# Kernel tuning notes

Measured on AMD Instinct MI355X. Metric: run time of the kernel, lower is better.

Reference implementation:

```python
import jax, jax.numpy as jnp
import numpy as np
import math

B, S, D, H = 1, 4096, 1024, 16
DH = D // H  # head_dim = 64
NEG = -10000.0  # matches torch masked-fill value in source (not -inf)


def setup_inputs() -> dict:
    key = jax.random.key(0)
    ks = jax.random.split(key, 5)
    scale = 0.02
    return {
        "x": jax.random.normal(ks[0], (B, S, D), dtype=jnp.float32),
        "Wqkv_w": jax.random.normal(ks[1], (3 * D, D), dtype=jnp.float32) * scale,
        "Wqkv_b": jax.random.normal(ks[2], (3 * D,), dtype=jnp.float32) * scale,
        "out_w": jax.random.normal(ks[3], (D, D), dtype=jnp.float32) * scale,
        "out_b": jax.random.normal(ks[4], (D,), dtype=jnp.float32) * scale,
    }


def reference(x, Wqkv_w, Wqkv_b, out_w, out_b):
    # QKV projection: (B,S,D) @ (D,3D) + b -> (B,S,3,H,DH)
    qkv = jnp.einsum('bsd,ed->bse', x, Wqkv_w) + Wqkv_b
    qkv = qkv.reshape(B, S, 3, H, DH)
    q, k, v = qkv[:, :, 0], qkv[:, :, 1], qkv[:, :, 2]  # each (B,S,H,DH)
    softmax_scale = 1.0 / math.sqrt(DH)
    # scores: (B,H,T,S)
    scores = jnp.einsum('bthd,bshd->bhts', q, k * softmax_scale)
    # causal additive mask with -10000 above diagonal (faithful to source)
    causal_mask = jnp.triu(jnp.full((S, S), NEG, dtype=scores.dtype), k=1)
    scores = scores + causal_mask
    attention = jax.nn.softmax(scores, axis=-1)
    context = jnp.einsum('bhts,bshd->bthd', attention, v)  # (B,T,H,DH)
    context = context.reshape(B, S, D)
    out = jnp.einsum('bsd,ed->bse', context, out_w) + out_b
    return out
```

## Files before the change

kernel.cpp:

```cpp
#include <hip/hip_runtime.h>
#include <hip/hip_bf16.h>

using f32x4  = __attribute__((ext_vector_type(4))) float;
using f32x16 = __attribute__((ext_vector_type(16))) float;
using bf16x8 = __attribute__((ext_vector_type(8))) __bf16;
using u16x8  = __attribute__((ext_vector_type(8))) unsigned short;
using u32x4  = __attribute__((ext_vector_type(4))) unsigned int;

#define DEV __device__ __forceinline__

constexpr int S_  = 4096;
constexpr int D_  = 1024;
constexpr int KD  = 1024;

constexpr size_t XB_OFF   = 0;
constexpr size_t WQKV_OFF = 8388608;
constexpr size_t WOUT_OFF = 14680064;
constexpr size_t QB_OFF   = 16777216;
constexpr size_t KB_OFF   = 25165824;
constexpr size_t VT_OFF   = 33554432;
constexpr size_t CTX_OFF  = 41943040;

DEV unsigned short f2bf(float f) {
  __hip_bfloat16 h = __float2bfloat16(f);
  return __builtin_bit_cast(unsigned short, h);
}

DEV void gl_lds16(const void* g, void* l) {
  __builtin_amdgcn_global_load_lds(
      (const __attribute__((address_space(1))) void*)g,
      (__attribute__((address_space(3))) void*)l, 16, 0, 0);
}

DEV f32x4 mfma16(bf16x8 a, bf16x8 b, f32x4 c) {
  return __builtin_amdgcn_mfma_f32_16x16x32_bf16(a, b, c, 0, 0, 0);
}
DEV f32x16 mfma32(bf16x8 a, bf16x8 b, f32x16 c) {
  return __builtin_amdgcn_mfma_f32_32x32x16_bf16(a, b, c, 0, 0, 0);
}
DEV unsigned cvtpk(float lo, float hi) {
  unsigned r;
  asm("v_cvt_pk_bf16_f32 %0, %1, %2" : "=v"(r) : "v"(lo), "v"(hi));
  return r;
}
DEV float exp2_fast(float x) {
  float r;
  asm("v_exp_f32 %0, %1" : "=v"(r) : "v"(x));
  return r;
}
DEV void pl32(unsigned& a, unsigned& b) {
  asm("v_permlane32_swap_b32 %0, %1" : "+v"(a), "+v"(b));
}
DEV float xhalf_max(float x) {
  float y;
  asm("v_mov_b32 %0, %1" : "=v"(y) : "v"(x));
  unsigned a = __builtin_bit_cast(unsigned, x), b = __builtin_bit_cast(unsigned, y);
  pl32(a, b);
  return fmaxf(__builtin_bit_cast(float, a), __builtin_bit_cast(float, b));
}
DEV float xhalf_add(float x) {
  float y;
  asm("v_mov_b32 %0, %1" : "=v"(y) : "v"(x));
  unsigned a = __builtin_bit_cast(unsigned, x), b = __builtin_bit_cast(unsigned, y);
  pl32(a, b);
  return __builtin_bit_cast(float, a) + __builtin_bit_cast(float, b);
}

__global__ void cvt_k(const float* __restrict__ s, unsigned short* __restrict__ d, int n8) {
  int i = blockIdx.x * 256 + threadIdx.x;
  if (i >= n8) return;
  const float4* s4 = (const float4*)s;
  float4 a = s4[2 * i], b = s4[2 * i + 1];
  u16x8 o;
  o[0] = f2bf(a.x); o[1] = f2bf(a.y); o[2] = f2bf(a.z); o[3] = f2bf(a.w);
  o[4] = f2bf(b.x); o[5] = f2bf(b.y); o[6] = f2bf(b.z); o[7] = f2bf(b.w);
  ((u16x8*)d)[i] = o;
}

template <int EPI>
__global__ __launch_bounds__(256)
void gemm_bt_k(const unsigned short* __restrict__ A,
               const unsigned short* __restrict__ Bt,
               const float* __restrict__ bias,
               unsigned short* __restrict__ qb,
               unsigned short* __restrict__ kb,
               unsigned short* __restrict__ vt,
               float* __restrict__ outf) {
  __shared__ unsigned short As[128 * 32];
  __shared__ unsigned short Bs[128 * 32];
  const int t = threadIdx.x;
  const int w = t >> 6, l = t & 63;
  const int lr = l & 15, lg = l >> 4, lk = lg * 8;
  const int m0 = blockIdx.y * 128, n0 = blockIdx.x * 128;
  const int wm = (w >> 1) * 64, wn = (w & 1) * 64;

  f32x4 acc[4][4] = {};

  const int srow = t >> 2;
  const int scolb = (t & 3) << 4;
  const char* Ag = (const char*)A + (size_t)(m0 + srow) * (KD * 2) + scolb;
  const char* Bg = (const char*)Bt + (size_t)(n0 + srow) * (KD * 2) + scolb;
  char* AsB = (char*)As;
  char* BsB = (char*)Bs;

  for (int kt = 0; kt < KD / 32; ++kt) {
    const char* ak = Ag + kt * 64;
    const char* bk = Bg + kt * 64;
    gl_lds16(ak,                 AsB + t * 16);
    gl_lds16(ak + 64 * (KD * 2), AsB + 4096 + t * 16);
    gl_lds16(bk,                 BsB + t * 16);
    gl_lds16(bk + 64 * (KD * 2), BsB + 4096 + t * 16);
    __syncthreads();

    bf16x8 a[4], b[4];
#pragma unroll
    for (int mi = 0; mi < 4; ++mi)
      a[mi] = *(const bf16x8*)&As[(wm + mi * 16 + lr) * 32 + lk];
#pragma unroll
    for (int ni = 0; ni < 4; ++ni)
      b[ni] = *(const bf16x8*)&Bs[(wn + ni * 16 + lr) * 32 + lk];
#pragma unroll
    for (int mi = 0; mi < 4; ++mi)
#pragma unroll
      for (int ni = 0; ni < 4; ++ni)
        acc[mi][ni] = mfma16(a[mi], b[ni], acc[mi][ni]);
    __syncthreads();
  }

  const int r0 = lg * 4;
  if (EPI == 0) {
    const int which = n0 >> 10;
    const float kscale = 0.125f * 1.44269504088896f;
#pragma unroll
    for (int mi = 0; mi < 4; ++mi) {
      const int sbase = m0 + wm + mi * 16 + r0;
#pragma unroll
      for (int ni = 0; ni < 4; ++ni) {
        const int e = n0 + wn + ni * 16 + lr;
        const float bv = bias[e];
        const int h = (e & 1023) >> 6, dd = e & 63;
#pragma unroll
        for (int r = 0; r < 4; ++r) {
          const float v = acc[mi][ni][r] + bv;
          const int sr = sbase + r;
          if (which == 0)      qb[((size_t)(h * S_ + sr)) * 64 + dd] = f2bf(v);
          else if (which == 1) kb[((size_t)(h * S_ + sr)) * 64 + dd] = f2bf(v * kscale);
          else                 vt[((size_t)(h * 64 + dd)) * S_ + sr] = f2bf(v);
        }
      }
    }
  } else {
#pragma unroll
    for (int mi = 0; mi < 4; ++mi) {
      const int sbase = m0 + wm + mi * 16 + r0;
#pragma unroll
      for (int ni = 0; ni < 4; ++ni) {
        const int e = n0 + wn + ni * 16 + lr;
        const float bv = bias[e];
#pragma unroll
        for (int r = 0; r < 4; ++r)
          outf[(size_t)(sbase + r) * D_ + e] = acc[mi][ni][r] + bv;
      }
    }
  }
}

__global__ __launch_bounds__(512, 2)
void attn_k(const unsigned short* __restrict__ Qb,
            const unsigned short* __restrict__ Kb,
            const unsigned short* __restrict__ Vt,
            unsigned short* __restrict__ ctx) {
  __shared__ char smem[65536];

  const int t = threadIdx.x;
  const int w8 = t >> 6;
  const int g  = w8 >> 2;
  const int w  = w8 & 3;
  const int l = t & 63, lq = l & 31, hi = l >> 5;
  const int pairIdx = blockIdx.x;
  const int h = blockIdx.y;

  const int sg = t >> 8;
  const int ts = t & 255;
  const int srow = ts >> 3;
  const int ssw  = ((ts & 7) << 4) ^ ((srow & 7) << 4);
  const char* Kg0 = (const char*)Kb + (size_t)(h * S_) * 128;
  const char* Vg0 = (const char*)Vt + (size_t)(h * 64) * (size_t)(S_ * 2);

  for (int task = 0; task < 2; ++task) {
    const int bi = task == 0 ? (31 - pairIdx) : pairIdx;
    const int q0 = bi * 128;
    const int qrow = q0 + w * 32 + lq;
    const int qwmin = q0 + w * 32, qwmax = qwmin + 31;
    const int niter = bi + 1;

    const unsigned short* Qr = Qb + ((size_t)(h * S_ + qrow)) * 64;
    bf16x8 qf[4];
#pragma unroll
    for (int d0 = 0; d0 < 4; ++d0)
      qf[d0] = *(const bf16x8*)(Qr + d0 * 16 + hi * 8);

    f32x16 cacc[2] = {};
    float m = -INFINITY, lsum = 0.f;

    auto stage = [&](int buf, int it) {
      const int kv0 = (it + sg * niter) * 64;
      char* kd = smem + sg * 16384 + buf * 8192;
      const char* Kg = Kg0 + (size_t)kv0 * 128;
      gl_lds16(Kg + (size_t)srow * 128 + ssw,        kd + ts * 16);
      gl_lds16(Kg + (size_t)(32 + srow) * 128 + ssw, kd + 4096 + ts * 16);
      char* vd = smem + 32768 + sg * 16384 + buf * 8192;
      const char* Vg = Vg0 + (size_t)kv0 * 2;
      gl_lds16(Vg + (size_t)srow * (S_ * 2) + ssw,        vd + ts * 16);
      gl_lds16(Vg + (size_t)(32 + srow) * (S_ * 2) + ssw, vd + 4096 + ts * 16);
    };

    int cur = 0;
    stage(0, 0);

    for (int it = 0; it < niter; ++it) {
      __syncthreads();
      if (it + 1 < niter) stage(cur ^ 1, it + 1);
      const char* Kt = smem + g * 16384 + cur * 8192;
      const char* Vl = smem + 32768 + g * 16384 + cur * 8192;
      const int tt = it + g * niter;

#pragma unroll
      for (int kvh = 0; kvh < 2; ++kvh) {
        const int kv0s = tt * 64 + kvh * 32;
        if (kv0s > qwmax) continue;

        f32x16 st = {};
        const int kr = kvh * 32 + lq;
        const char* kbase = Kt + kr * 128;
        const int ksw = (kr & 7) << 4;
#pragma unroll
        for (int d0 = 0; d0 < 4; ++d0) {
          bf16x8 kf = *(const bf16x8*)(kbase + ((d0 * 32 + hi * 16) ^ ksw));
          st = mfma32(kf, qf[d0], st);
        }

        if (kv0s + 31 > qwmin) {
#pragma unroll
          for (int r = 0; r < 16; ++r) {
            const int kvg = kv0s + (r & 3) + 8 * (r >> 2) + 4 * hi;
            if (kvg > qrow) st[r] = -INFINITY;
          }
        }

        float pmax = st[0];
#pragma unroll
        for (int r = 1; r < 16; ++r) pmax = fmaxf(pmax, st[r]);
        pmax = xhalf_max(pmax);

        if (!__all(pmax <= m)) {
          const float mnew = fmaxf(m, pmax);
          const float alpha = exp2_fast(m - mnew);
          lsum *= alpha;
#pragma unroll
          for (int j = 0; j < 16; ++j) { cacc[0][j] *= alpha; cacc[1][j] *= alpha; }
          m = mnew;
        }

        float p[16];
        float rs = 0.f;
#pragma unroll
        for (int r = 0; r < 16; ++r) { p[r] = exp2_fast(st[r] - m); rs += p[r]; }
        lsum += xhalf_add(rs);

        unsigned x0 = cvtpk(p[0], p[1]),  x1 = cvtpk(p[2], p[3]);
        unsigned y0 = cvtpk(p[4], p[5]),  y1 = cvtpk(p[6], p[7]);
        pl32(x0, y0); pl32(x1, y1);
        u32x4 f0 = {x0, x1, y0, y1};
        bf16x8 pf0 = __builtin_bit_cast(bf16x8, f0);
        unsigned x2 = cvtpk(p[8], p[9]),   x3 = cvtpk(p[10], p[11]);
        unsigned y2 = cvtpk(p[12], p[13]), y3 = cvtpk(p[14], p[15]);
        pl32(x2, y2); pl32(x3, y3);
        u32x4 f1 = {x2, x3, y2, y3};
        bf16x8 pf1 = __builtin_bit_cast(bf16x8, f1);

#pragma unroll
        for (int db = 0; db < 2; ++db) {
          const int dr = db * 32 + lq;
          const char* vbase = Vl + dr * 128;
          const int vsw = (dr & 7) << 4;
          bf16x8 v0 = *(const bf16x8*)(vbase + ((kvh * 64 + hi * 16) ^ vsw));
          bf16x8 v1 = *(const bf16x8*)(vbase + ((kvh * 64 + 32 + hi * 16) ^ vsw));
          cacc[db] = mfma32(v0, pf0, cacc[db]);
          cacc[db] = mfma32(v1, pf1, cacc[db]);
        }
      }
      cur ^= 1;
    }

    __syncthreads();
    float* comb = (float*)smem;
    float* slot = comb + (size_t)(w * 64 + l) * 36;
    if (g == 1) {
      slot[0] = m; slot[1] = lsum;
#pragma unroll
      for (int j = 0; j < 16; ++j) { slot[4 + j] = cacc[0][j]; slot[20 + j] = cacc[1][j]; }
    }
    __syncthreads();
    if (g == 0) {
      const float m1 = slot[0], l1 = slot[1];
      const float M = fmaxf(m, m1);
      const float a0 = exp2_fast(m - M), a1 = exp2_fast(m1 - M);
      const float inv = 1.0f / (lsum * a0 + l1 * a1);
      const float s0 = a0 * inv, s1 = a1 * inv;
      unsigned short* base = ctx + (size_t)qrow * D_ + h * 64;
#pragma unroll
      for (int db = 0; db < 2; ++db)
#pragma unroll
        for (int r = 0; r < 16; r += 2) {
          const float o0 = cacc[db][r]     * s0 + slot[4 + db * 16 + r]     * s1;
          const float o1 = cacc[db][r + 1] * s0 + slot[4 + db * 16 + r + 1] * s1;
          const unsigned wv = cvtpk(o0, o1);
          const int d = (r & 3) + 8 * (r >> 2) + 4 * hi + 32 * db;
          *(unsigned*)(base + d) = wv;
        }
    }
    __syncthreads();
  }
}

extern "C" void kernel_launch(void* const* d_in, const int* in_sizes, int n_in,
                              void* d_out, int out_size, void* d_ws, size_t ws_size,
                              hipStream_t stream) {
  const float* x      = (const float*)d_in[0];
  const float* Wqkv_w = (const float*)d_in[1];
  const float* Wqkv_b = (const float*)d_in[2];
  const float* out_w  = (const float*)d_in[3];
  const float* out_b  = (const float*)d_in[4];
  float* out = (float*)d_out;
  char* ws = (char*)d_ws;

  unsigned short* xb    = (unsigned short*)(ws + XB_OFF);
  unsigned short* wqkvb = (unsigned short*)(ws + WQKV_OFF);
  unsigned short* woutb = (unsigned short*)(ws + WOUT_OFF);
  unsigned short* Qb    = (unsigned short*)(ws + QB_OFF);
  unsigned short* Kb    = (unsigned short*)(ws + KB_OFF);
  unsigned short* Vt    = (unsigned short*)(ws + VT_OFF);
  unsigned short* ctx   = (unsigned short*)(ws + CTX_OFF);

  cvt_k<<<2048, 256, 0, stream>>>(x, xb, 4096 * 1024 / 8);
  cvt_k<<<1536, 256, 0, stream>>>(Wqkv_w, wqkvb, 3072 * 1024 / 8);
  cvt_k<<<512, 256, 0, stream>>>(out_w, woutb, 1024 * 1024 / 8);

  gemm_bt_k<0><<<dim3(24, 32), 256, 0, stream>>>(xb, wqkvb, Wqkv_b, Qb, Kb, Vt, nullptr);

  attn_k<<<dim3(16, 16), 512, 0, stream>>>(Qb, Kb, Vt, ctx);

  gemm_bt_k<1><<<dim3(8, 32), 256, 0, stream>>>(ctx, woutb, out_b, nullptr, nullptr, nullptr, out);
}
```

Baseline: 139.2 us.

## Double-buffer GEMMs, merge conversions, split proj tiles, interleave attention KV halves

Merges the three fp32-to-bf16 conversion launches into one grid-stride kernel to cut launch overhead. Both GEMMs now double-buffer their LDS tiles so the next k-slice loads while the current one is computed, which also removes one barrier per iteration. The output projection uses 128x64 tiles, doubling its block count to fill more CUs. The attention kernel now gives the two wave groups interleaved KV tiles instead of contiguous halves, so causal-masked work is spread more evenly between them, and it guards the merge step against an all-masked group (-inf max). The added shared-memory use and extra blocks change occupancy.

```diff
diff --git a/kernel.cpp b/kernel.cpp
--- a/kernel.cpp
+++ b/kernel.cpp
@@ -66,28 +66,35 @@
   return __builtin_bit_cast(float, a) + __builtin_bit_cast(float, b);
 }
 
-__global__ void cvt_k(const float* __restrict__ s, unsigned short* __restrict__ d, int n8) {
-  int i = blockIdx.x * 256 + threadIdx.x;
-  if (i >= n8) return;
-  const float4* s4 = (const float4*)s;
-  float4 a = s4[2 * i], b = s4[2 * i + 1];
-  u16x8 o;
-  o[0] = f2bf(a.x); o[1] = f2bf(a.y); o[2] = f2bf(a.z); o[3] = f2bf(a.w);
-  o[4] = f2bf(b.x); o[5] = f2bf(b.y); o[6] = f2bf(b.z); o[7] = f2bf(b.w);
-  ((u16x8*)d)[i] = o;
-}
-
-template <int EPI>
+__global__ void cvt_all_k(const float* __restrict__ x,
+                          const float* __restrict__ wq,
+                          const float* __restrict__ wo,
+                          unsigned short* __restrict__ xb,
+                          unsigned short* __restrict__ wqb,
+                          unsigned short* __restrict__ wob) {
+  for (int u = blockIdx.x * 256 + threadIdx.x; u < 1048576; u += 2048 * 256) {
+    const float* s; unsigned short* d; int off;
+    if (u < 524288)      { s = x;  d = xb;  off = u; }
+    else if (u < 917504) { s = wq; d = wqb; off = u - 524288; }
+    else                 { s = wo; d = wob; off = u - 917504; }
+    const float4* s4 = (const float4*)s;
+    float4 a = s4[2 * off], b = s4[2 * off + 1];
+    u16x8 o;
+    o[0] = f2bf(a.x); o[1] = f2bf(a.y); o[2] = f2bf(a.z); o[3] = f2bf(a.w);
+    o[4] = f2bf(b.x); o[5] = f2bf(b.y); o[6] = f2bf(b.z); o[7] = f2bf(b.w);
+    ((u16x8*)d)[off] = o;
+  }
+}
+
 __global__ __launch_bounds__(256)
-void gemm_bt_k(const unsigned short* __restrict__ A,
-               const unsigned short* __restrict__ Bt,
-               const float* __restrict__ bias,
-               unsigned short* __restrict__ qb,
-               unsigned short* __restrict__ kb,
-               unsigned short* __restrict__ vt,
-               float* __restrict__ outf) {
-  __shared__ unsigned short As[128 * 32];
-  __shared__ unsigned short Bs[128 * 32];
+void gemm_qkv_k(const unsigned short* __restrict__ A,
+                const unsigned short* __restrict__ Bt,
+                const float* __restrict__ bias,
+                unsigned short* __restrict__ qb,
+                unsigned short* __restrict__ kb,
+                unsigned short* __restrict__ vt) {
+  __shared__ unsigned short As[2][4096];
+  __shared__ unsigned short Bs[2][4096];
   const int t = threadIdx.x;
   const int w = t >> 6, l = t & 63;
   const int lr = l & 15, lg = l >> 4, lk = lg * 8;
@@ -100,67 +107,120 @@
   const int scolb = (t & 3) << 4;
   const char* Ag = (const char*)A + (size_t)(m0 + srow) * (KD * 2) + scolb;
   const char* Bg = (const char*)Bt + (size_t)(n0 + srow) * (KD * 2) + scolb;
-  char* AsB = (char*)As;
-  char* BsB = (char*)Bs;
-
-  for (int kt = 0; kt < KD / 32; ++kt) {
+
+  auto stage = [&](int buf, int kt) {
     const char* ak = Ag + kt * 64;
     const char* bk = Bg + kt * 64;
+    char* AsB = (char*)&As[buf][0];
+    char* BsB = (char*)&Bs[buf][0];
     gl_lds16(ak,                 AsB + t * 16);
     gl_lds16(ak + 64 * (KD * 2), AsB + 4096 + t * 16);
     gl_lds16(bk,                 BsB + t * 16);
     gl_lds16(bk + 64 * (KD * 2), BsB + 4096 + t * 16);
+  };
+
+  stage(0, 0);
+  for (int kt = 0; kt < KD / 32; ++kt) {
     __syncthreads();
+    if (kt + 1 < KD / 32) stage((kt + 1) & 1, kt + 1);
+    const int buf = kt & 1;
 
     bf16x8 a[4], b[4];
 #pragma unroll
     for (int mi = 0; mi < 4; ++mi)
-      a[mi] = *(const bf16x8*)&As[(wm + mi * 16 + lr) * 32 + lk];
+      a[mi] = *(const bf16x8*)&As[buf][(wm + mi * 16 + lr) * 32 + lk];
 #pragma unroll
     for (int ni = 0; ni < 4; ++ni)
-      b[ni] = *(const bf16x8*)&Bs[(wn + ni * 16 + lr) * 32 + lk];
+      b[ni] = *(const bf16x8*)&Bs[buf][(wn + ni * 16 + lr) * 32 + lk];
 #pragma unroll
     for (int mi = 0; mi < 4; ++mi)
 #pragma unroll
       for (int ni = 0; ni < 4; ++ni)
         acc[mi][ni] = mfma16(a[mi], b[ni], acc[mi][ni]);
-    __syncthreads();
   }
 
   const int r0 = lg * 4;
-  if (EPI == 0) {
-    const int which = n0 >> 10;
-    const float kscale = 0.125f * 1.44269504088896f;
-#pragma unroll
-    for (int mi = 0; mi < 4; ++mi) {
-      const int sbase = m0 + wm + mi * 16 + r0;
-#pragma unroll
-      for (int ni = 0; ni < 4; ++ni) {
-        const int e = n0 + wn + ni * 16 + lr;
-        const float bv = bias[e];
-        const int h = (e & 1023) >> 6, dd = e & 63;
-#pragma unroll
-        for (int r = 0; r < 4; ++r) {
-          const float v = acc[mi][ni][r] + bv;
-          const int sr = sbase + r;
-          if (which == 0)      qb[((size_t)(h * S_ + sr)) * 64 + dd] = f2bf(v);
-          else if (which == 1) kb[((size_t)(h * S_ + sr)) * 64 + dd] = f2bf(v * kscale);
-          else                 vt[((size_t)(h * 64 + dd)) * S_ + sr] = f2bf(v);
-        }
+  const int which = n0 >> 10;
+  const float kscale = 0.125f * 1.44269504088896f;
+#pragma unroll
+  for (int mi = 0; mi < 4; ++mi) {
+    const int sbase = m0 + wm + mi * 16 + r0;
+#pragma unroll
+    for (int ni = 0; ni < 4; ++ni) {
+      const int e = n0 + wn + ni * 16 + lr;
+      const float bv = bias[e];
+      const int h = (e & 1023) >> 6, dd = e & 63;
+#pragma unroll
+      for (int r = 0; r < 4; ++r) {
+        const float v = acc[mi][ni][r] + bv;
+        const int sr = sbase + r;
+        if (which == 0)      qb[((size_t)(h * S_ + sr)) * 64 + dd] = f2bf(v);
+        else if (which == 1) kb[((size_t)(h * S_ + sr)) * 64 + dd] = f2bf(v * kscale);
+        else                 vt[((size_t)(h * 64 + dd)) * S_ + sr] = f2bf(v);
       }
     }
-  } else {
-#pragma unroll
-    for (int mi = 0; mi < 4; ++mi) {
-      const int sbase = m0 + wm + mi * 16 + r0;
-#pragma unroll
-      for (int ni = 0; ni < 4; ++ni) {
-        const int e = n0 + wn + ni * 16 + lr;
-        const float bv = bias[e];
-#pragma unroll
-        for (int r = 0; r < 4; ++r)
-          outf[(size_t)(sbase + r) * D_ + e] = acc[mi][ni][r] + bv;
-      }
+  }
+}
+
+__global__ __launch_bounds__(256)
+void gemm_proj_k(const unsigned short* __restrict__ A,
+                 const unsigned short* __restrict__ Bt,
+                 const float* __restrict__ bias,
+                 float* __restrict__ outf) {
+  __shared__ unsigned short As[2][4096];
+  __shared__ unsigned short Bs[2][2048];
+  const int t = threadIdx.x;
+  const int w = t >> 6, l = t & 63;
+  const int lr = l & 15, lg = l >> 4, lk = lg * 8;
+  const int m0 = blockIdx.y * 128, n0 = blockIdx.x * 64;
+  const int wm = (w >> 1) * 64, wn = (w & 1) * 32;
+
+  f32x4 acc[4][2] = {};
+
+  const int srow = t >> 2;
+  const int scolb = (t & 3) << 4;
+  const char* Ag = (const char*)A + (size_t)(m0 + srow) * (KD * 2) + scolb;
+  const char* Bg = (const char*)Bt + (size_t)(n0 + (t >> 2)) * (KD * 2) + scolb;
+
+  auto stage = [&](int buf, int kt) {
+    const char* ak = Ag + kt * 64;
+    char* AsB = (char*)&As[buf][0];
+    gl_lds16(ak,                 AsB + t * 16);
+    gl_lds16(ak + 64 * (KD * 2), AsB + 4096 + t * 16);
+    gl_lds16(Bg + kt * 64, (char*)&Bs[buf][0] + t * 16);
+  };
+
+  stage(0, 0);
+  for (int kt = 0; kt < KD / 32; ++kt) {
+    __syncthreads();
+    if (kt + 1 < KD / 32) stage((kt + 1) & 1, kt + 1);
+    const int buf = kt & 1;
+
+    bf16x8 a[4], b[2];
+#pragma unroll
+    for (int mi = 0; mi < 4; ++mi)
+      a[mi] = *(const bf16x8*)&As[buf][(wm + mi * 16 + lr) * 32 + lk];
+#pragma unroll
+    for (int ni = 0; ni < 2; ++ni)
+      b[ni] = *(const bf16x8*)&Bs[buf][(wn + ni * 16 + lr) * 32 + lk];
+#pragma unroll
+    for (int mi = 0; mi < 4; ++mi)
+#pragma unroll
+      for (int ni = 0; ni < 2; ++ni)
+        acc[mi][ni] = mfma16(a[mi], b[ni], acc[mi][ni]);
+  }
+
+  const int r0 = lg * 4;
+#pragma unroll
+  for (int mi = 0; mi < 4; ++mi) {
+    const int sbase = m0 + wm + mi * 16 + r0;
+#pragma unroll
+    for (int ni = 0; ni < 2; ++ni) {
+      const int e = n0 + wn + ni * 16 + lr;
+      const float bv = bias[e];
+#pragma unroll
+      for (int r = 0; r < 4; ++r)
+        outf[(size_t)(sbase + r) * D_ + e] = acc[mi][ni][r] + bv;
     }
   }
 }
@@ -192,6 +252,7 @@
     const int q0 = bi * 128;
     const int qrow = q0 + w * 32 + lq;
     const int qwmin = q0 + w * 32, qwmax = qwmin + 31;
+    const int ntiles = 2 * bi + 2;
     const int niter = bi + 1;
 
     const unsigned short* Qr = Qb + ((size_t)(h * S_ + qrow)) * 64;
@@ -203,8 +264,8 @@
     f32x16 cacc[2] = {};
     float m = -INFINITY, lsum = 0.f;
 
-    auto stage = [&](int buf, int it) {
-      const int kv0 = (it + sg * niter) * 64;
+    auto stage = [&](int buf, int tl) {
+      const int kv0 = tl * 64;
       char* kd = smem + sg * 16384 + buf * 8192;
       const char* Kg = Kg0 + (size_t)kv0 * 128;
       gl_lds16(Kg + (size_t)srow * 128 + ssw,        kd + ts * 16);
@@ -216,18 +277,18 @@
     };
 
     int cur = 0;
-    stage(0, 0);
+    stage(0, sg);
 
     for (int it = 0; it < niter; ++it) {
       __syncthreads();
-      if (it + 1 < niter) stage(cur ^ 1, it + 1);
+      if (2 * (it + 1) + sg < ntiles) stage(cur ^ 1, 2 * (it + 1) + sg);
       const char* Kt = smem + g * 16384 + cur * 8192;
       const char* Vl = smem + 32768 + g * 16384 + cur * 8192;
-      const int tt = it + g * niter;
+      const int tl = 2 * it + g;
 
 #pragma unroll
       for (int kvh = 0; kvh < 2; ++kvh) {
-        const int kv0s = tt * 64 + kvh * 32;
+        const int kv0s = tl * 64 + kvh * 32;
         if (kv0s > qwmax) continue;
 
         f32x16 st = {};
@@ -262,19 +323,18 @@
           m = mnew;
         }
 
-        float p[16];
         float rs = 0.f;
 #pragma unroll
-        for (int r = 0; r < 16; ++r) { p[r] = exp2_fast(st[r] - m); rs += p[r]; }
+        for (int r = 0; r < 16; ++r) { st[r] = exp2_fast(st[r] - m); rs += st[r]; }
         lsum += xhalf_add(rs);
 
-        unsigned x0 = cvtpk(p[0], p[1]),  x1 = cvtpk(p[2], p[3]);
-        unsigned y0 = cvtpk(p[4], p[5]),  y1 = cvtpk(p[6], p[7]);
+        unsigned x0 = cvtpk(st[0], st[1]),   x1 = cvtpk(st[2], st[3]);
+        unsigned y0 = cvtpk(st[4], st[5]),   y1 = cvtpk(st[6], st[7]);
         pl32(x0, y0); pl32(x1, y1);
         u32x4 f0 = {x0, x1, y0, y1};
         bf16x8 pf0 = __builtin_bit_cast(bf16x8, f0);
-        unsigned x2 = cvtpk(p[8], p[9]),   x3 = cvtpk(p[10], p[11]);
-        unsigned y2 = cvtpk(p[12], p[13]), y3 = cvtpk(p[14], p[15]);
+        unsigned x2 = cvtpk(st[8], st[9]),   x3 = cvtpk(st[10], st[11]);
+        unsigned y2 = cvtpk(st[12], st[13]), y3 = cvtpk(st[14], st[15]);
         pl32(x2, y2); pl32(x3, y3);
         u32x4 f1 = {x2, x3, y2, y3};
         bf16x8 pf1 = __builtin_bit_cast(bf16x8, f1);
@@ -305,7 +365,8 @@
     if (g == 0) {
       const float m1 = slot[0], l1 = slot[1];
       const float M = fmaxf(m, m1);
-      const float a0 = exp2_fast(m - M), a1 = exp2_fast(m1 - M);
+      const float a0 = (m  == -INFINITY) ? 0.f : exp2_fast(m - M);
+      const float a1 = (m1 == -INFINITY) ? 0.f : exp2_fast(m1 - M);
       const float inv = 1.0f / (lsum * a0 + l1 * a1);
       const float s0 = a0 * inv, s1 = a1 * inv;
       unsigned short* base = ctx + (size_t)qrow * D_ + h * 64;
@@ -343,13 +404,11 @@
   unsigned short* Vt    = (unsigned short*)(ws + VT_OFF);
   unsigned short* ctx   = (unsigned short*)(ws + CTX_OFF);
 
-  cvt_k<<<2048, 256, 0, stream>>>(x, xb, 4096 * 1024 / 8);
-  cvt_k<<<1536, 256, 0, stream>>>(Wqkv_w, wqkvb, 3072 * 1024 / 8);
-  cvt_k<<<512, 256, 0, stream>>>(out_w, woutb, 1024 * 1024 / 8);
-
-  gemm_bt_k<0><<<dim3(24, 32), 256, 0, stream>>>(xb, wqkvb, Wqkv_b, Qb, Kb, Vt, nullptr);
+  cvt_all_k<<<2048, 256, 0, stream>>>(x, Wqkv_w, out_w, xb, wqkvb, woutb);
+
+  gemm_qkv_k<<<dim3(24, 32), 256, 0, stream>>>(xb, wqkvb, Wqkv_b, Qb, Kb, Vt);
 
   attn_k<<<dim3(16, 16), 512, 0, stream>>>(Qb, Kb, Vt, ctx);
 
-  gemm_bt_k<1><<<dim3(8, 32), 256, 0, stream>>>(ctx, woutb, out_b, nullptr, nullptr, nullptr, out);
-}
+  gemm_proj_k<<<dim3(16, 32), 256, 0, stream>>>(ctx, woutb, out_b, out);
+}
```

After: 145.2 us. 1.04x slower.
